# Kernel optimization log

Measured on AMD Instinct MI355X. Metric: run time of the kernel, lower is better.

## Reference

```python
import jax, jax.numpy as jnp
import numpy as np

B, T, D = 2, 2048, 1024
H = 16
HD = D // H
EPS = 1e-6


def rmsnorm(x, w):
    # x: [..., HD]
    var = jnp.mean(x * x, axis=-1, keepdims=True)
    return x * jax.lax.rsqrt(var + EPS) * w


def setup_inputs() -> dict:
    key = jax.random.key(0)
    ks = jax.random.split(key, 12)
    s = 1.0 / np.sqrt(D)
    return {
        "query": jax.random.normal(ks[0], (B, T, D), jnp.float32),
        "key_value": jax.random.normal(ks[1], (B, T, D), jnp.float32),
        "Wq": jax.random.normal(ks[2], (D, D), jnp.float32) * s,
        "bq": jnp.zeros((D,), jnp.float32),
        "Wk": jax.random.normal(ks[3], (D, D), jnp.float32) * s,
        "bk": jnp.zeros((D,), jnp.float32),
        "Wv": jax.random.normal(ks[4], (D, D), jnp.float32) * s,
        "bv": jnp.zeros((D,), jnp.float32),
        "Wo": jax.random.normal(ks[5], (D, D), jnp.float32) * s,
        "bo": jnp.zeros((D,), jnp.float32),
        "qn_w": jnp.ones((HD,), jnp.float32),
        "kn_w": jnp.ones((HD,), jnp.float32),
    }


def reference(query, key_value, Wq, bq, Wk, bk, Wv, bv, Wo, bo, qn_w, kn_w):
    scale = HD ** -0.5
    # projections -> [B, H, T, HD]
    def split_heads(x):
        return x.reshape(B, T, H, HD).transpose(0, 2, 1, 3)
    q = split_heads(query @ Wq.T + bq)
    k = split_heads(key_value @ Wk.T + bk)
    v = split_heads(key_value @ Wv.T + bv)
    q = rmsnorm(q, qn_w)
    k = rmsnorm(k, kn_w)
    attn = jnp.einsum('bhqd,bhkd->bhqk', q, k) * scale  # [B,H,T,T]
    attn = jax.nn.softmax(attn, axis=-1)
    out = jnp.einsum('bhqk,bhkd->bhqd', attn, v)
    out = out.transpose(0, 2, 1, 3).reshape(B, T, D)
    return out @ Wo.T + bo
```

## Files before the change

kernel.cpp:

```cpp
#include <hip/hip_runtime.h>
#include <stdint.h>

#define Bb 2
#define Tt 2048
#define Dd 1024
#define Hh 16
#define HDd 64
#define Mm 4096

typedef __attribute__((ext_vector_type(4))) float f32x4;
typedef __attribute__((ext_vector_type(16))) float f32x16;
typedef __attribute__((ext_vector_type(8))) __bf16 bf16x8;
typedef __attribute__((ext_vector_type(8))) short s16x8;
typedef __attribute__((ext_vector_type(4))) float fvec4;
typedef __attribute__((ext_vector_type(4))) unsigned int u32x4;

__device__ __forceinline__ float bf2f(ushort u){
  union { unsigned int i; float f; } v; v.i = ((unsigned int)u) << 16; return v.f;
}
__device__ __forceinline__ ushort f2bf(float f){
  union { float f; unsigned int i; } v; v.f = f;
  unsigned int u = v.i;
  u += 0x7FFFu + ((u >> 16) & 1u);
  return (ushort)(u >> 16);
}

__device__ __forceinline__ void gload16(const void* g, void* l){
  __builtin_amdgcn_global_load_lds(
      (const __attribute__((address_space(1))) void*)g,
      (__attribute__((address_space(3))) void*)l, 16, 0, 0);
}

__global__ __launch_bounds__(256) void cvt_all(
    const float* __restrict__ q, const float* __restrict__ kv,
    const float* __restrict__ wq, const float* __restrict__ wk,
    const float* __restrict__ wv, const float* __restrict__ wo,
    ushort* __restrict__ oq, ushort* __restrict__ okv, ushort* __restrict__ owq,
    ushort* __restrict__ owk, ushort* __restrict__ owv, ushort* __restrict__ owo)
{
  const int NQ = Mm*Dd/4;
  const int NW = Dd*Dd/4;
  int j = blockIdx.x * 256 + threadIdx.x;
  const float* s; ushort* d;
  if (j < NQ)            { s = q;  d = oq;  }
  else if ((j -= NQ) < NQ){ s = kv; d = okv; }
  else if ((j -= NQ) < NW){ s = wq; d = owq; }
  else if ((j -= NW) < NW){ s = wk; d = owk; }
  else if ((j -= NW) < NW){ s = wv; d = owv; }
  else        { j -= NW;   s = wo; d = owo; }
  fvec4 v = ((const fvec4*)s)[j];
  unsigned int lo = (unsigned int)f2bf(v.x) | ((unsigned int)f2bf(v.y) << 16);
  unsigned int hi = (unsigned int)f2bf(v.z) | ((unsigned int)f2bf(v.w) << 16);
  ((uint2*)d)[j] = make_uint2(lo, hi);
}

template<int MODE>
__device__ __forceinline__ void proj_body(char* smem,
    const ushort* __restrict__ A, const ushort* __restrict__ W,
    const float* __restrict__ bias, const float* __restrict__ nw, float rmsScale,
    ushort* __restrict__ Oh, int m0, int n0)
{
  ushort* As = (ushort*)smem;
  ushort* Bs = (ushort*)(smem + 16384);
  const int tid  = threadIdx.x;
  const int w    = tid >> 6, lid = tid & 63;
  const int lrow = lid & 15, g = lid >> 4;
  const int wm   = w << 5;

  f32x4 acc[2][4] = {};

  for (int kt = 0; kt < Dd; kt += 64){
    __syncthreads();
    #pragma unroll
    for (int i = 0; i < 4; ++i){
      int e   = tid + i*256;
      int row = e >> 3;
      int c   = (e & 7) ^ (row & 7);
      gload16(A + (size_t)(m0 + row)*Dd + kt + c*8, &As[e*8]);
    }
    #pragma unroll
    for (int i = 0; i < 2; ++i){
      int e   = tid + i*256;
      int row = e >> 3;
      int c   = (e & 7) ^ (row & 7);
      gload16(W + (size_t)(n0 + row)*Dd + kt + c*8, &Bs[e*8]);
    }
    __syncthreads();
    #pragma unroll
    for (int kc = 0; kc < 2; ++kc){
      bf16x8 af[2], bfr[4];
      #pragma unroll
      for (int r = 0; r < 2; ++r){
        int row = wm + r*16 + lrow;
        af[r] = *(const bf16x8*)&As[row*64 + (((kc*4 + g) ^ (row & 7)) << 3)];
      }
      #pragma unroll
      for (int c = 0; c < 4; ++c){
        int row = c*16 + lrow;
        bfr[c] = *(const bf16x8*)&Bs[row*64 + (((kc*4 + g) ^ (row & 7)) << 3)];
      }
      #pragma unroll
      for (int r = 0; r < 2; ++r)
        #pragma unroll
        for (int c = 0; c < 4; ++c)
          acc[r][c] = __builtin_amdgcn_mfma_f32_16x16x32_bf16(af[r], bfr[c], acc[r][c], 0, 0, 0);
    }
  }
  float bv[4], wv4[4];
  #pragma unroll
  for (int c = 0; c < 4; ++c){
    bv[c] = bias[n0 + c*16 + lrow];
    if (MODE == 1) wv4[c] = nw[c*16 + lrow];
  }
  #pragma unroll
  for (int r = 0; r < 2; ++r){
    #pragma unroll
    for (int b = 0; b < 4; ++b){
      float v[4];
      #pragma unroll
      for (int c = 0; c < 4; ++c) v[c] = acc[r][c][b] + bv[c];
      float sc = 1.0f;
      if (MODE == 1){
        float ss = v[0]*v[0] + v[1]*v[1] + v[2]*v[2] + v[3]*v[3];
        ss += __shfl_xor(ss, 1, 64);
        ss += __shfl_xor(ss, 2, 64);
        ss += __shfl_xor(ss, 4, 64);
        ss += __shfl_xor(ss, 8, 64);
        sc = rsqrtf(ss * (1.0f/64.0f) + 1e-6f) * rmsScale;
      }
      int row = m0 + wm + r*16 + g*4 + b;
      #pragma unroll
      for (int c = 0; c < 4; ++c){
        int col = n0 + c*16 + lrow;
        if (MODE == 1) Oh[(size_t)row*Dd + col] = f2bf(v[c] * sc * wv4[c]);
        else           Oh[(size_t)row*Dd + col] = f2bf(v[c]);
      }
    }
  }
}

__global__ __launch_bounds__(256) void gemm_qkv(
  const ushort* __restrict__ qbf, const ushort* __restrict__ kvbf,
  const ushort* __restrict__ wq, const ushort* __restrict__ wk, const ushort* __restrict__ wv,
  const float* __restrict__ bq, const float* __restrict__ bk, const float* __restrict__ bv,
  const float* __restrict__ qnw, const float* __restrict__ knw,
  ushort* __restrict__ Q, ushort* __restrict__ Kx, ushort* __restrict__ V)
{
  __shared__ char smem[24576];
  int bid  = (blockIdx.x & 7) * 192 + (blockIdx.x >> 3);
  int proj = bid >> 9;
  int rem  = bid & 511;
  int mt   = rem >> 4, nt = rem & 15;
  if (proj == 0)
    proj_body<1>(smem, qbf, wq, bq, qnw, 0.18033688011112042f, Q, mt*128, nt*64);
  else if (proj == 1)
    proj_body<1>(smem, kvbf, wk, bk, knw, 1.0f, Kx, mt*128, nt*64);
  else
    proj_body<0>(smem, kvbf, wv, bv, nullptr, 1.0f, V, mt*128, nt*64);
}

__global__ __launch_bounds__(256) void gemm_o(
  const ushort* __restrict__ X, const ushort* __restrict__ wo,
  const float* __restrict__ bo, float* __restrict__ out)
{
  __shared__ char smem[24576];
  ushort* As = (ushort*)smem;
  ushort* Bs = (ushort*)(smem + 16384);
  int bid = (blockIdx.x & 7) * 64 + (blockIdx.x >> 3);
  const int mt = bid >> 4, nt = bid & 15;
  const int m0 = mt*128, n0 = nt*64;

  const int tid  = threadIdx.x;
  const int w    = tid >> 6, lid = tid & 63;
  const int lrow = lid & 15, g = lid >> 4;
  const int wm   = (w >> 1) << 6, wn = (w & 1) << 5;

  f32x4 acc[4][2] = {};

  for (int kt = 0; kt < Dd; kt += 64){
    __syncthreads();
    #pragma unroll
    for (int i = 0; i < 4; ++i){
      int e   = tid + i*256;
      int row = e >> 3;
      int c   = (e & 7) ^ (row & 7);
      gload16(X + (size_t)(m0 + row)*Dd + kt + c*8, &As[e*8]);
    }
    #pragma unroll
    for (int i = 0; i < 2; ++i){
      int e   = tid + i*256;
      int row = e >> 3;
      int c   = (e & 7) ^ (row & 7);
      gload16(wo + (size_t)(n0 + row)*Dd + kt + c*8, &Bs[e*8]);
    }
    __syncthreads();
    #pragma unroll
    for (int kc = 0; kc < 2; ++kc){
      bf16x8 af[4], bfr[2];
      #pragma unroll
      for (int r = 0; r < 4; ++r){
        int row = wm + r*16 + lrow;
        af[r] = *(const bf16x8*)&As[row*64 + (((kc*4 + g) ^ (row & 7)) << 3)];
      }
      #pragma unroll
      for (int c = 0; c < 2; ++c){
        int row = wn + c*16 + lrow;
        bfr[c] = *(const bf16x8*)&Bs[row*64 + (((kc*4 + g) ^ (row & 7)) << 3)];
      }
      #pragma unroll
      for (int r = 0; r < 4; ++r)
        #pragma unroll
        for (int c = 0; c < 2; ++c)
          acc[r][c] = __builtin_amdgcn_mfma_f32_16x16x32_bf16(af[r], bfr[c], acc[r][c], 0, 0, 0);
    }
  }
  const int colbase = n0 + wn;
  float bv[2];
  #pragma unroll
  for (int c = 0; c < 2; ++c) bv[c] = bo[colbase + c*16 + lrow];
  #pragma unroll
  for (int r = 0; r < 4; ++r){
    #pragma unroll
    for (int b = 0; b < 4; ++b){
      int row = m0 + wm + r*16 + g*4 + b;
      #pragma unroll
      for (int c = 0; c < 2; ++c){
        int col = colbase + c*16 + lrow;
        out[(size_t)row*Dd + col] = acc[r][c][b] + bv[c];
      }
    }
  }
}

__global__ __launch_bounds__(256, 2) void attn_k(
  const ushort* __restrict__ Qb, const ushort* __restrict__ Kb,
  const ushort* __restrict__ Vb, ushort* __restrict__ Ob)
{
  __shared__ char L[65536];

  const int tid  = threadIdx.x;
  const int w    = tid >> 6, lid = tid & 63;
  const int half = w >> 1,  qw = w & 1;
  const int c31  = lid & 31, hi = lid >> 5;
  const int ti   = tid & 127;

  int bid = blockIdx.x;
  int wg  = (bid & 7) * 64 + (bid >> 3);
  int bh  = wg >> 4, qt = wg & 15;
  int bb  = bh >> 4, hh = bh & 15;
  const size_t base = (size_t)bb * Tt * Dd + (size_t)hh * HDd;

  bf16x8 qf[2][4];
  #pragma unroll
  for (int sub = 0; sub < 2; ++sub)
    #pragma unroll
    for (int kc = 0; kc < 4; ++kc)
      qf[sub][kc] = *(const bf16x8*)&Qb[base + (size_t)(qt*128 + qw*64 + sub*32 + c31)*Dd + kc*16 + hi*8];

  char* Kl = L + half*32768;
  char* Vl = Kl + 16384;

  int kfo[2][4];
  #pragma unroll
  for (int kh = 0; kh < 2; ++kh)
    #pragma unroll
    for (int kc = 0; kc < 4; ++kc)
      kfo[kh][kc] = (kh*32 + c31)*128 + (((2*kc + hi) ^ (c31 & 7)) << 4);

  int vfo[2][4];
  #pragma unroll
  for (int dh = 0; dh < 2; ++dh){
    int d = dh*32 + c31, F = ((d >> 3) ^ d) & 7;
    #pragma unroll
    for (int kcp = 0; kcp < 4; ++kcp)
      vfo[dh][kcp] = d*128 + (((2*kcp + hi) ^ F) << 4);
  }

  const int d0 = (ti & 7) * 8, key0 = (ti >> 3) * 4;
  int vso[8];
  {
    int m  = key0 >> 2;
    int c  = ((m >> 2) << 1) | (m & 1);
    int hb = ((m >> 1) & 1) * 8;
    #pragma unroll
    for (int dd = 0; dd < 8; ++dd){
      int d = d0 + dd, F = ((d >> 3) ^ d) & 7;
      vso[dd] = d*128 + ((c ^ F) << 4) + hb;
    }
  }

  const ushort* ksg[4]; char* kdst[4];
  #pragma unroll
  for (int i = 0; i < 4; ++i){
    int e = ti + i*128;
    int row = e >> 3, cc = (e & 7) ^ (row & 7);
    ksg[i]  = Kb + base + (size_t)(half*1024 + row) * Dd + cc*8;
    kdst[i] = Kl + e*16;
  }
  const ushort* vsg = Vb + base + (size_t)(half*1024 + key0) * Dd + d0;
  const size_t kstep = (size_t)64 * Dd;

  #pragma unroll
  for (int i = 0; i < 4; ++i) gload16(ksg[i], kdst[i]);
  u32x4 vv0 = *(const u32x4*)(vsg);
  u32x4 vv1 = *(const u32x4*)(vsg + Dd);
  u32x4 vv2 = *(const u32x4*)(vsg + 2*Dd);
  u32x4 vv3 = *(const u32x4*)(vsg + 3*Dd);
  #pragma unroll
  for (int i = 0; i < 4; ++i) ksg[i] += kstep;
  vsg += kstep;

  f32x16 o[2][2] = {};
  f32x16 lacc[2] = {};
  const __bf16 one1 = (__bf16)1.0f;
  const bf16x8 ones = {one1, one1, one1, one1, one1, one1, one1, one1};

  auto vscatter = [&](int bufoff){
    #pragma unroll
    for (int dd = 0; dd < 8; ++dd){
      unsigned sel = (dd & 1) ? 0x07060302u : 0x05040100u;
      unsigned lo  = __builtin_amdgcn_perm(vv1[dd >> 1], vv0[dd >> 1], sel);
      unsigned hi2 = __builtin_amdgcn_perm(vv3[dd >> 1], vv2[dd >> 1], sel);
      *(uint2*)(Vl + vso[dd] + bufoff) = make_uint2(lo, hi2);
    }
  };

  auto dosm = [&](f32x16* s, bf16x8* pao){
    #pragma unroll
    for (int kh = 0; kh < 2; ++kh)
      #pragma unroll
      for (int i = 0; i < 16; ++i)
        s[kh][i] = __builtin_amdgcn_exp2f(s[kh][i]);
    #pragma unroll
    for (int kh = 0; kh < 2; ++kh)
      #pragma unroll
      for (int c = 0; c < 2; ++c){
        unsigned u0, u1, u2, u3;
        asm("v_cvt_pk_bf16_f32 %0, %1, %2" : "=v"(u0) : "v"(s[kh][8*c+0]), "v"(s[kh][8*c+1]));
        asm("v_cvt_pk_bf16_f32 %0, %1, %2" : "=v"(u1) : "v"(s[kh][8*c+2]), "v"(s[kh][8*c+3]));
        asm("v_cvt_pk_bf16_f32 %0, %1, %2" : "=v"(u2) : "v"(s[kh][8*c+4]), "v"(s[kh][8*c+5]));
        asm("v_cvt_pk_bf16_f32 %0, %1, %2" : "=v"(u3) : "v"(s[kh][8*c+6]), "v"(s[kh][8*c+7]));
        u32x4 uu = {u0, u1, u2, u3};
        pao[kh*2 + c] = __builtin_bit_cast(bf16x8, uu);
      }
  };

#define ATTN_TILE(BUF, PREFETCH)                                                     \
  {                                                                                  \
    vscatter((BUF)*8192);                                                            \
    __syncthreads();                                                                 \
    if (PREFETCH){                                                                   \
      _Pragma("unroll")                                                              \
      for (int i = 0; i < 4; ++i){                                                   \
        gload16(ksg[i], kdst[i] + ((BUF)^1)*8192);                                   \
        ksg[i] += kstep;                                                             \
      }                                                                              \
      vv0 = *(const u32x4*)(vsg);                                                    \
      vv1 = *(const u32x4*)(vsg + Dd);                                               \
      vv2 = *(const u32x4*)(vsg + 2*Dd);                                             \
      vv3 = *(const u32x4*)(vsg + 3*Dd);                                             \
      vsg += kstep;                                                                  \
    }                                                                                \
    f32x16 s0[2] = {}, s1[2] = {};                                                   \
    __builtin_amdgcn_s_setprio(1);                                                   \
    _Pragma("unroll")                                                                \
    for (int kh = 0; kh < 2; ++kh)                                                   \
      _Pragma("unroll")                                                              \
      for (int kc = 0; kc < 4; ++kc){                                                \
        bf16x8 kf = *(const bf16x8*)(Kl + kfo[kh][kc] + (BUF)*8192);                 \
        s0[kh] = __builtin_amdgcn_mfma_f32_32x32x16_bf16(kf, qf[0][kc], s0[kh], 0,0,0); \
        s1[kh] = __builtin_amdgcn_mfma_f32_32x32x16_bf16(kf, qf[1][kc], s1[kh], 0,0,0); \
      }                                                                              \
    __builtin_amdgcn_s_setprio(0);                                                   \
    bf16x8 pa0[4], pa1[4];                                                           \
    dosm(s0, pa0);                                                                   \
    dosm(s1, pa1);                                                                   \
    __builtin_amdgcn_s_setprio(1);                                                   \
    _Pragma("unroll")                                                                \
    for (int dh = 0; dh < 2; ++dh)                                                   \
      _Pragma("unroll")                                                              \
      for (int kcp = 0; kcp < 4; ++kcp){                                             \
        bf16x8 vf = *(const bf16x8*)(Vl + vfo[dh][kcp] + (BUF)*8192);                \
        o[0][dh] = __builtin_amdgcn_mfma_f32_32x32x16_bf16(vf, pa0[kcp], o[0][dh], 0,0,0); \
        o[1][dh] = __builtin_amdgcn_mfma_f32_32x32x16_bf16(vf, pa1[kcp], o[1][dh], 0,0,0); \
      }                                                                              \
    _Pragma("unroll")                                                                \
    for (int kcp = 0; kcp < 4; ++kcp){                                               \
      lacc[0] = __builtin_amdgcn_mfma_f32_32x32x16_bf16(ones, pa0[kcp], lacc[0], 0,0,0); \
      lacc[1] = __builtin_amdgcn_mfma_f32_32x32x16_bf16(ones, pa1[kcp], lacc[1], 0,0,0); \
    }                                                                                \
    __builtin_amdgcn_s_setprio(0);                                                   \
  }

  for (int kt2 = 0; kt2 < 8; ++kt2){
    ATTN_TILE(0, true);
    ATTN_TILE(1, (kt2 != 7));
  }
#undef ATTN_TILE

  __syncthreads();
  if (half == 1){
    #pragma unroll
    for (int sub = 0; sub < 2; ++sub)
      #pragma unroll
      for (int dh = 0; dh < 2; ++dh)
        #pragma unroll
        for (int G = 0; G < 4; ++G){
          f32x4 v = { o[sub][dh][4*G+0], o[sub][dh][4*G+1], o[sub][dh][4*G+2], o[sub][dh][4*G+3] };
          *(f32x4*)(L + (((sub*8 + dh*4 + G)*128) + ti)*16) = v;
        }
    f32x4 ml = {lacc[0][0], lacc[1][0], 0.f, 0.f};
    *(f32x4*)(L + ((16*128) + ti)*16) = ml;
  }
  __syncthreads();
  if (half == 0){
    f32x4 ml = *(const f32x4*)(L + ((16*128) + ti)*16);
    #pragma unroll
    for (int sub = 0; sub < 2; ++sub){
      float inv = 1.0f / (lacc[sub][0] + ml[sub]);
      int qrow = qt*128 + qw*64 + sub*32 + c31;
      #pragma unroll
      for (int dh = 0; dh < 2; ++dh)
        #pragma unroll
        for (int G = 0; G < 4; ++G){
          f32x4 op = *(const f32x4*)(L + (((sub*8 + dh*4 + G)*128) + ti)*16);
          float oc0 = (o[sub][dh][4*G+0] + op[0]) * inv;
          float oc1 = (o[sub][dh][4*G+1] + op[1]) * inv;
          float oc2 = (o[sub][dh][4*G+2] + op[2]) * inv;
          float oc3 = (o[sub][dh][4*G+3] + op[3]) * inv;
          uint2 u;
          u.x = (unsigned)f2bf(oc0) | ((unsigned)f2bf(oc1) << 16);
          u.y = (unsigned)f2bf(oc2) | ((unsigned)f2bf(oc3) << 16);
          *(uint2*)&Ob[base + (size_t)qrow*Dd + dh*32 + 8*G + hi*4] = u;
        }
    }
  }
}

extern "C" void kernel_launch(void* const* d_in, const int* in_sizes, int n_in,
                              void* d_out, int out_size, void* d_ws, size_t ws_size,
                              hipStream_t stream)
{
  const float* query = (const float*)d_in[0];
  const float* keyv  = (const float*)d_in[1];
  const float* Wq    = (const float*)d_in[2];
  const float* bq    = (const float*)d_in[3];
  const float* Wk    = (const float*)d_in[4];
  const float* bk    = (const float*)d_in[5];
  const float* Wv    = (const float*)d_in[6];
  const float* bv    = (const float*)d_in[7];
  const float* Wo    = (const float*)d_in[8];
  const float* bo    = (const float*)d_in[9];
  const float* qnw   = (const float*)d_in[10];
  const float* knw   = (const float*)d_in[11];
  float* out = (float*)d_out;

  char* p = (char*)d_ws;
  ushort* qbf  = (ushort*)p; p += (size_t)Mm*Dd*2;
  ushort* kvbf = (ushort*)p; p += (size_t)Mm*Dd*2;
  ushort* wqb  = (ushort*)p; p += (size_t)Dd*Dd*2;
  ushort* wkb  = (ushort*)p; p += (size_t)Dd*Dd*2;
  ushort* wvb  = (ushort*)p; p += (size_t)Dd*Dd*2;
  ushort* wob  = (ushort*)p; p += (size_t)Dd*Dd*2;
  ushort* Qb   = (ushort*)p; p += (size_t)Mm*Dd*2;
  ushort* Kbf  = (ushort*)p; p += (size_t)Mm*Dd*2;
  ushort* Vbf  = (ushort*)p; p += (size_t)Mm*Dd*2;
  ushort* Ab   = (ushort*)p; p += (size_t)Mm*Dd*2;

  cvt_all<<<dim3(12288), dim3(256), 0, stream>>>(query, keyv, Wq, Wk, Wv, Wo,
                                                 qbf, kvbf, wqb, wkb, wvb, wob);

  gemm_qkv<<<dim3(1536), dim3(256), 0, stream>>>(qbf, kvbf, wqb, wkb, wvb,
                                                 bq, bk, bv, qnw, knw, Qb, Kbf, Vbf);

  attn_k<<<dim3(512), dim3(256), 0, stream>>>(Qb, Kbf, Vbf, Ab);

  gemm_o<<<dim3(512), dim3(256), 0, stream>>>(Ab, wob, bo, out);
}
```

Before: 116.5 us.

## Fuse fp32-to-bf16 activation conversion into QKV projection GEMM A-tile loads

Removes the separate conversion pass over query and key_value. The QKV GEMM now reads fp32 activations directly into registers, converts them with packed bf16 instructions, and stores them to LDS, prefetching the next k-tile into registers while the MFMAs run. This avoids writing and re-reading two bf16 activation buffers. In exchange, each GEMM tile reads twice the bytes of A, and K and V blocks both reread the same fp32 key_value, with more register pressure and a synchronous register-staged load path.

```diff
diff --git a/kernel.cpp b/kernel.cpp
--- a/kernel.cpp
+++ b/kernel.cpp
@@ -31,20 +31,16 @@
       (__attribute__((address_space(3))) void*)l, 16, 0, 0);
 }
 
-__global__ __launch_bounds__(256) void cvt_all(
-    const float* __restrict__ q, const float* __restrict__ kv,
+__global__ __launch_bounds__(256) void cvt_w(
     const float* __restrict__ wq, const float* __restrict__ wk,
     const float* __restrict__ wv, const float* __restrict__ wo,
-    ushort* __restrict__ oq, ushort* __restrict__ okv, ushort* __restrict__ owq,
-    ushort* __restrict__ owk, ushort* __restrict__ owv, ushort* __restrict__ owo)
-{
-  const int NQ = Mm*Dd/4;
+    ushort* __restrict__ owq, ushort* __restrict__ owk,
+    ushort* __restrict__ owv, ushort* __restrict__ owo)
+{
   const int NW = Dd*Dd/4;
   int j = blockIdx.x * 256 + threadIdx.x;
   const float* s; ushort* d;
-  if (j < NQ)            { s = q;  d = oq;  }
-  else if ((j -= NQ) < NQ){ s = kv; d = okv; }
-  else if ((j -= NQ) < NW){ s = wq; d = owq; }
+  if (j < NW)            { s = wq; d = owq; }
   else if ((j -= NW) < NW){ s = wk; d = owk; }
   else if ((j -= NW) < NW){ s = wv; d = owv; }
   else        { j -= NW;   s = wo; d = owo; }
@@ -56,7 +52,7 @@
 
 template<int MODE>
 __device__ __forceinline__ void proj_body(char* smem,
-    const ushort* __restrict__ A, const ushort* __restrict__ W,
+    const float* __restrict__ Af, const ushort* __restrict__ W,
     const float* __restrict__ bias, const float* __restrict__ nw, float rmsScale,
     ushort* __restrict__ Oh, int m0, int n0)
 {
@@ -68,16 +64,39 @@
   const int wm   = w << 5;
 
   f32x4 acc[2][4] = {};
+  u32x4 apk[4];
+
+  const float* asrc[4];
+  #pragma unroll
+  for (int i = 0; i < 4; ++i){
+    int e = tid + i*256;
+    int row = e >> 3, c = (e & 7) ^ (row & 7);
+    asrc[i] = Af + (size_t)(m0 + row)*Dd + c*8;
+  }
+
+  auto loadA = [&](int kt){
+    #pragma unroll
+    for (int i = 0; i < 4; ++i){
+      const float* src = asrc[i] + kt;
+      fvec4 f0 = *(const fvec4*)src;
+      fvec4 f1 = *(const fvec4*)(src + 4);
+      unsigned w0, w1, w2, w3;
+      asm("v_cvt_pk_bf16_f32 %0, %1, %2" : "=v"(w0) : "v"(f0.x), "v"(f0.y));
+      asm("v_cvt_pk_bf16_f32 %0, %1, %2" : "=v"(w1) : "v"(f0.z), "v"(f0.w));
+      asm("v_cvt_pk_bf16_f32 %0, %1, %2" : "=v"(w2) : "v"(f1.x), "v"(f1.y));
+      asm("v_cvt_pk_bf16_f32 %0, %1, %2" : "=v"(w3) : "v"(f1.z), "v"(f1.w));
+      u32x4 p = {w0, w1, w2, w3};
+      apk[i] = p;
+    }
+  };
+
+  loadA(0);
 
   for (int kt = 0; kt < Dd; kt += 64){
     __syncthreads();
     #pragma unroll
-    for (int i = 0; i < 4; ++i){
-      int e   = tid + i*256;
-      int row = e >> 3;
-      int c   = (e & 7) ^ (row & 7);
-      gload16(A + (size_t)(m0 + row)*Dd + kt + c*8, &As[e*8]);
-    }
+    for (int i = 0; i < 4; ++i)
+      *(u32x4*)&As[(tid + i*256)*8] = apk[i];
     #pragma unroll
     for (int i = 0; i < 2; ++i){
       int e   = tid + i*256;
@@ -86,6 +105,7 @@
       gload16(W + (size_t)(n0 + row)*Dd + kt + c*8, &Bs[e*8]);
     }
     __syncthreads();
+    if (kt + 64 < Dd) loadA(kt + 64);
     #pragma unroll
     for (int kc = 0; kc < 2; ++kc){
       bf16x8 af[2], bfr[4];
@@ -140,7 +160,7 @@
 }
 
 __global__ __launch_bounds__(256) void gemm_qkv(
-  const ushort* __restrict__ qbf, const ushort* __restrict__ kvbf,
+  const float* __restrict__ query, const float* __restrict__ keyv,
   const ushort* __restrict__ wq, const ushort* __restrict__ wk, const ushort* __restrict__ wv,
   const float* __restrict__ bq, const float* __restrict__ bk, const float* __restrict__ bv,
   const float* __restrict__ qnw, const float* __restrict__ knw,
@@ -152,11 +172,11 @@
   int rem  = bid & 511;
   int mt   = rem >> 4, nt = rem & 15;
   if (proj == 0)
-    proj_body<1>(smem, qbf, wq, bq, qnw, 0.18033688011112042f, Q, mt*128, nt*64);
+    proj_body<1>(smem, query, wq, bq, qnw, 0.18033688011112042f, Q, mt*128, nt*64);
   else if (proj == 1)
-    proj_body<1>(smem, kvbf, wk, bk, knw, 1.0f, Kx, mt*128, nt*64);
+    proj_body<1>(smem, keyv, wk, bk, knw, 1.0f, Kx, mt*128, nt*64);
   else
-    proj_body<0>(smem, kvbf, wv, bv, nullptr, 1.0f, V, mt*128, nt*64);
+    proj_body<0>(smem, keyv, wv, bv, nullptr, 1.0f, V, mt*128, nt*64);
 }
 
 __global__ __launch_bounds__(256) void gemm_o(
@@ -456,8 +476,6 @@
   float* out = (float*)d_out;
 
   char* p = (char*)d_ws;
-  ushort* qbf  = (ushort*)p; p += (size_t)Mm*Dd*2;
-  ushort* kvbf = (ushort*)p; p += (size_t)Mm*Dd*2;
   ushort* wqb  = (ushort*)p; p += (size_t)Dd*Dd*2;
   ushort* wkb  = (ushort*)p; p += (size_t)Dd*Dd*2;
   ushort* wvb  = (ushort*)p; p += (size_t)Dd*Dd*2;
@@ -467,10 +485,9 @@
   ushort* Vbf  = (ushort*)p; p += (size_t)Mm*Dd*2;
   ushort* Ab   = (ushort*)p; p += (size_t)Mm*Dd*2;
 
-  cvt_all<<<dim3(12288), dim3(256), 0, stream>>>(query, keyv, Wq, Wk, Wv, Wo,
-                                                 qbf, kvbf, wqb, wkb, wvb, wob);
-
-  gemm_qkv<<<dim3(1536), dim3(256), 0, stream>>>(qbf, kvbf, wqb, wkb, wvb,
+  cvt_w<<<dim3(4096), dim3(256), 0, stream>>>(Wq, Wk, Wv, Wo, wqb, wkb, wvb, wob);
+
+  gemm_qkv<<<dim3(1536), dim3(256), 0, stream>>>(query, keyv, wqb, wkb, wvb,
                                                  bq, bk, bv, qnw, knw, Qb, Kbf, Vbf);
 
   attn_k<<<dim3(512), dim3(256), 0, stream>>>(Qb, Kbf, Vbf, Ab);
```

Result: slower. 123.6 us (+6.1%).

## Halve attention query tile and single-buffer V to raise occupancy

Applied to the files above, without the earlier changes.

The attention kernel now processes 64 query rows per block instead of 128, doubling the grid to 1024 blocks. Each wave handles one 32-row Q subtile, which reduces register pressure. V is single-buffered in LDS with an extra barrier per tile, shrinking shared memory from 64KB to 48KB, and launch bounds allow 3 blocks per CU. The goal is more resident waves and better latency hiding. The cost is that each K/V tile is reused over half as many queries, doubling K/V traffic, plus one extra synchronization per tile.

```diff
diff --git a/kernel.cpp b/kernel.cpp
--- a/kernel.cpp
+++ b/kernel.cpp
@@ -232,11 +232,11 @@
   }
 }
 
-__global__ __launch_bounds__(256, 2) void attn_k(
+__global__ __launch_bounds__(256, 3) void attn_k(
   const ushort* __restrict__ Qb, const ushort* __restrict__ Kb,
   const ushort* __restrict__ Vb, ushort* __restrict__ Ob)
 {
-  __shared__ char L[65536];
+  __shared__ char L[49152];
 
   const int tid  = threadIdx.x;
   const int w    = tid >> 6, lid = tid & 63;
@@ -245,19 +245,17 @@
   const int ti   = tid & 127;
 
   int bid = blockIdx.x;
-  int wg  = (bid & 7) * 64 + (bid >> 3);
-  int bh  = wg >> 4, qt = wg & 15;
+  int wg  = (bid & 7) * 128 + (bid >> 3);
+  int bh  = wg >> 5, qt = wg & 31;
   int bb  = bh >> 4, hh = bh & 15;
   const size_t base = (size_t)bb * Tt * Dd + (size_t)hh * HDd;
 
-  bf16x8 qf[2][4];
-  #pragma unroll
-  for (int sub = 0; sub < 2; ++sub)
-    #pragma unroll
-    for (int kc = 0; kc < 4; ++kc)
-      qf[sub][kc] = *(const bf16x8*)&Qb[base + (size_t)(qt*128 + qw*64 + sub*32 + c31)*Dd + kc*16 + hi*8];
-
-  char* Kl = L + half*32768;
+  bf16x8 qf[4];
+  #pragma unroll
+  for (int kc = 0; kc < 4; ++kc)
+    qf[kc] = *(const bf16x8*)&Qb[base + (size_t)(qt*64 + qw*32 + c31)*Dd + kc*16 + hi*8];
+
+  char* Kl = L + half*24576;
   char* Vl = Kl + 16384;
 
   int kfo[2][4];
@@ -310,18 +308,18 @@
   for (int i = 0; i < 4; ++i) ksg[i] += kstep;
   vsg += kstep;
 
-  f32x16 o[2][2] = {};
-  f32x16 lacc[2] = {};
+  f32x16 o[2] = {};
+  f32x16 lacc = {};
   const __bf16 one1 = (__bf16)1.0f;
   const bf16x8 ones = {one1, one1, one1, one1, one1, one1, one1, one1};
 
-  auto vscatter = [&](int bufoff){
+  auto vscatter = [&](){
     #pragma unroll
     for (int dd = 0; dd < 8; ++dd){
       unsigned sel = (dd & 1) ? 0x07060302u : 0x05040100u;
       unsigned lo  = __builtin_amdgcn_perm(vv1[dd >> 1], vv0[dd >> 1], sel);
       unsigned hi2 = __builtin_amdgcn_perm(vv3[dd >> 1], vv2[dd >> 1], sel);
-      *(uint2*)(Vl + vso[dd] + bufoff) = make_uint2(lo, hi2);
+      *(uint2*)(Vl + vso[dd]) = make_uint2(lo, hi2);
     }
   };
 
@@ -347,8 +345,8 @@
 
 #define ATTN_TILE(BUF, PREFETCH)                                                     \
   {                                                                                  \
-    vscatter((BUF)*8192);                                                            \
-    __syncthreads();                                                                 \
+    vscatter();                           \
+    __syncthreads();                      \
     if (PREFETCH){                                                                   \
       _Pragma("unroll")                                                              \
       for (int i = 0; i < 4; ++i){                                                   \
@@ -361,35 +359,31 @@
       vv3 = *(const u32x4*)(vsg + 3*Dd);                                             \
       vsg += kstep;                                                                  \
     }                                                                                \
-    f32x16 s0[2] = {}, s1[2] = {};                                                   \
+    f32x16 s0[2] = {};                                                               \
     __builtin_amdgcn_s_setprio(1);                                                   \
     _Pragma("unroll")                                                                \
     for (int kh = 0; kh < 2; ++kh)                                                   \
       _Pragma("unroll")                                                              \
       for (int kc = 0; kc < 4; ++kc){                                                \
         bf16x8 kf = *(const bf16x8*)(Kl + kfo[kh][kc] + (BUF)*8192);                 \
-        s0[kh] = __builtin_amdgcn_mfma_f32_32x32x16_bf16(kf, qf[0][kc], s0[kh], 0,0,0); \
-        s1[kh] = __builtin_amdgcn_mfma_f32_32x32x16_bf16(kf, qf[1][kc], s1[kh], 0,0,0); \
+        s0[kh] = __builtin_amdgcn_mfma_f32_32x32x16_bf16(kf, qf[kc], s0[kh], 0,0,0); \
       }                                                                              \
     __builtin_amdgcn_s_setprio(0);                                                   \
-    bf16x8 pa0[4], pa1[4];                                                           \
+    bf16x8 pa0[4];                                                                   \
     dosm(s0, pa0);                                                                   \
-    dosm(s1, pa1);                                                                   \
     __builtin_amdgcn_s_setprio(1);                                                   \
     _Pragma("unroll")                                                                \
     for (int dh = 0; dh < 2; ++dh)                                                   \
       _Pragma("unroll")                                                              \
       for (int kcp = 0; kcp < 4; ++kcp){                                             \
-        bf16x8 vf = *(const bf16x8*)(Vl + vfo[dh][kcp] + (BUF)*8192);                \
-        o[0][dh] = __builtin_amdgcn_mfma_f32_32x32x16_bf16(vf, pa0[kcp], o[0][dh], 0,0,0); \
-        o[1][dh] = __builtin_amdgcn_mfma_f32_32x32x16_bf16(vf, pa1[kcp], o[1][dh], 0,0,0); \
+        bf16x8 vf = *(const bf16x8*)(Vl + vfo[dh][kcp]);                             \
+        o[dh] = __builtin_amdgcn_mfma_f32_32x32x16_bf16(vf, pa0[kcp], o[dh], 0,0,0); \
       }                                                                              \
     _Pragma("unroll")                                                                \
-    for (int kcp = 0; kcp < 4; ++kcp){                                               \
-      lacc[0] = __builtin_amdgcn_mfma_f32_32x32x16_bf16(ones, pa0[kcp], lacc[0], 0,0,0); \
-      lacc[1] = __builtin_amdgcn_mfma_f32_32x32x16_bf16(ones, pa1[kcp], lacc[1], 0,0,0); \
-    }                                                                                \
+    for (int kcp = 0; kcp < 4; ++kcp)                                                \
+      lacc = __builtin_amdgcn_mfma_f32_32x32x16_bf16(ones, pa0[kcp], lacc, 0,0,0);   \
     __builtin_amdgcn_s_setprio(0);                                                   \
+    __syncthreads();                     \
   }
 
   for (int kt2 = 0; kt2 < 8; ++kt2){
@@ -398,42 +392,36 @@
   }
 #undef ATTN_TILE
 
-  __syncthreads();
   if (half == 1){
     #pragma unroll
-    for (int sub = 0; sub < 2; ++sub)
-      #pragma unroll
-      for (int dh = 0; dh < 2; ++dh)
-        #pragma unroll
-        for (int G = 0; G < 4; ++G){
-          f32x4 v = { o[sub][dh][4*G+0], o[sub][dh][4*G+1], o[sub][dh][4*G+2], o[sub][dh][4*G+3] };
-          *(f32x4*)(L + (((sub*8 + dh*4 + G)*128) + ti)*16) = v;
-        }
-    f32x4 ml = {lacc[0][0], lacc[1][0], 0.f, 0.f};
-    *(f32x4*)(L + ((16*128) + ti)*16) = ml;
+    for (int dh = 0; dh < 2; ++dh)
+      #pragma unroll
+      for (int G = 0; G < 4; ++G){
+        f32x4 v = { o[dh][4*G+0], o[dh][4*G+1], o[dh][4*G+2], o[dh][4*G+3] };
+        *(f32x4*)(L + (((dh*4 + G)*128) + ti)*16) = v;
+      }
+    f32x4 ml = {lacc[0], 0.f, 0.f, 0.f};
+    *(f32x4*)(L + ((8*128) + ti)*16) = ml;
   }
   __syncthreads();
   if (half == 0){
-    f32x4 ml = *(const f32x4*)(L + ((16*128) + ti)*16);
-    #pragma unroll
-    for (int sub = 0; sub < 2; ++sub){
-      float inv = 1.0f / (lacc[sub][0] + ml[sub]);
-      int qrow = qt*128 + qw*64 + sub*32 + c31;
-      #pragma unroll
-      for (int dh = 0; dh < 2; ++dh)
-        #pragma unroll
-        for (int G = 0; G < 4; ++G){
-          f32x4 op = *(const f32x4*)(L + (((sub*8 + dh*4 + G)*128) + ti)*16);
-          float oc0 = (o[sub][dh][4*G+0] + op[0]) * inv;
-          float oc1 = (o[sub][dh][4*G+1] + op[1]) * inv;
-          float oc2 = (o[sub][dh][4*G+2] + op[2]) * inv;
-          float oc3 = (o[sub][dh][4*G+3] + op[3]) * inv;
-          uint2 u;
-          u.x = (unsigned)f2bf(oc0) | ((unsigned)f2bf(oc1) << 16);
-          u.y = (unsigned)f2bf(oc2) | ((unsigned)f2bf(oc3) << 16);
-          *(uint2*)&Ob[base + (size_t)qrow*Dd + dh*32 + 8*G + hi*4] = u;
-        }
-    }
+    f32x4 ml = *(const f32x4*)(L + ((8*128) + ti)*16);
+    float inv = 1.0f / (lacc[0] + ml[0]);
+    int qrow = qt*64 + qw*32 + c31;
+    #pragma unroll
+    for (int dh = 0; dh < 2; ++dh)
+      #pragma unroll
+      for (int G = 0; G < 4; ++G){
+        f32x4 op = *(const f32x4*)(L + (((dh*4 + G)*128) + ti)*16);
+        float oc0 = (o[dh][4*G+0] + op[0]) * inv;
+        float oc1 = (o[dh][4*G+1] + op[1]) * inv;
+        float oc2 = (o[dh][4*G+2] + op[2]) * inv;
+        float oc3 = (o[dh][4*G+3] + op[3]) * inv;
+        uint2 u;
+        u.x = (unsigned)f2bf(oc0) | ((unsigned)f2bf(oc1) << 16);
+        u.y = (unsigned)f2bf(oc2) | ((unsigned)f2bf(oc3) << 16);
+        *(uint2*)&Ob[base + (size_t)qrow*Dd + dh*32 + 8*G + hi*4] = u;
+      }
   }
 }
 
@@ -473,7 +461,7 @@
   gemm_qkv<<<dim3(1536), dim3(256), 0, stream>>>(qbf, kvbf, wqb, wkb, wvb,
                                                  bq, bk, bv, qnw, knw, Qb, Kbf, Vbf);
 
-  attn_k<<<dim3(512), dim3(256), 0, stream>>>(Qb, Kbf, Vbf, Ab);
+  attn_k<<<dim3(1024), dim3(256), 0, stream>>>(Qb, Kbf, Vbf, Ab);
 
   gemm_o<<<dim3(512), dim3(256), 0, stream>>>(Ab, wob, bo, out);
 }
```

New measurement: 124.7 us. +7.1%, slower.
